# Optimization experiments

Hardware: AMD Instinct MI355X
Metric: run time of the kernel (lower is better)

Reference implementation:

```python
import jax, jax.numpy as jnp
import numpy as np

B, S, D = 2, 2048, 2048
HQ, HKV, HD = 16, 8, 128
F = 8192
V = 32000
L = 2
SW = 512
SOFTCAP = 50.0
THETA = 10000.0
EPS = 1e-6
LAYER_TYPES = ("sliding_attention", "full_attention")
SCALE = HD ** -0.5


def _rms_norm(x, w):
    # Gemma-style RMSNorm: fp32 compute, (1 + weight) scale
    x32 = x.astype(jnp.float32)
    n = x32 * jax.lax.rsqrt(jnp.mean(x32 * x32, axis=-1, keepdims=True) + EPS)
    return (n * (1.0 + w.astype(jnp.float32))).astype(x.dtype)


def _rotate_half(x):
    x1, x2 = jnp.split(x, 2, axis=-1)
    return jnp.concatenate([-x2, x1], axis=-1)


def _rope_cos_sin(position_ids):
    inv_freq = 1.0 / (THETA ** (jnp.arange(0, HD, 2, dtype=jnp.float32) / HD))  # [HD/2]
    freqs = position_ids.astype(jnp.float32)[..., None] * inv_freq  # [B,S,HD/2]
    emb = jnp.concatenate([freqs, freqs], axis=-1)  # [B,S,HD]
    return jnp.cos(emb), jnp.sin(emb)


def _apply_rope(q, k, cos, sin):
    # q,k: [B,H,S,HD]; cos,sin: [B,S,HD] -> unsqueeze head dim
    c, s = cos[:, None], sin[:, None]
    return q * c + _rotate_half(q) * s, k * c + _rotate_half(k) * s


def _build_masks(attention_mask, position_ids):
    key_mask = attention_mask.astype(bool)  # [B,S]
    # segment ids from position resets (packed sequences)
    boundaries = (position_ids[:, 1:] <= position_ids[:, :-1]).astype(jnp.int32)
    seg = jnp.cumsum(jnp.concatenate([jnp.ones((B, 1), jnp.int32), boundaries], axis=1), axis=1)
    block = seg[:, :, None] == seg[:, None, :]  # [B,S,S]
    full = (key_mask[:, None, :] & block)[:, None]  # [B,1,S,S]
    rows = jnp.arange(S)
    dist = rows[:, None] - rows[None, :]
    left = (SW + 1) // 2
    right = SW // 2 + 1
    window = ((dist >= 0) & (dist < left)) | ((dist < 0) & (-dist < right))
    sliding = full & window[None, None]
    return {"full_attention": full, "sliding_attention": sliding}


def _attention(x, l, wq, wk, wv, wo, q_norm_w, k_norm_w, cos, sin, mask):
    q = jnp.einsum("bsd,dhe->bhse", x, wq[l].reshape(D, HQ, HD))
    k = jnp.einsum("bsd,dhe->bhse", x, wk[l].reshape(D, HKV, HD))
    v = jnp.einsum("bsd,dhe->bhse", x, wv[l].reshape(D, HKV, HD))
    q = _rms_norm(q, q_norm_w[l])
    k = _rms_norm(k, k_norm_w[l])
    q, k = _apply_rope(q, k, cos, sin)
    rep = HQ // HKV
    k = jnp.repeat(k, rep, axis=1)  # repeat_kv
    v = jnp.repeat(v, rep, axis=1)
    scores = jnp.einsum("bhqd,bhkd->bhqk", q, k) * SCALE
    scores = jnp.tanh(scores / SOFTCAP) * SOFTCAP  # logit softcapping
    big_neg = jnp.finfo(jnp.float32).min
    scores = jnp.where(mask, scores, big_neg)
    probs = jax.nn.softmax(scores.astype(jnp.float32), axis=-1).astype(x.dtype)
    out = jnp.einsum("bhqk,bhkd->bhqd", probs, v)
    out = out.transpose(0, 2, 1, 3).reshape(B, S, HQ * HD)
    return out @ wo[l]


def _mlp(x, l, w_gate_up, w_down):
    gu = x @ w_gate_up[l]
    gate, up = jnp.split(gu, 2, axis=-1)
    return (jax.nn.gelu(gate, approximate=True) * up) @ w_down[l]


def setup_inputs() -> dict:
    key = jax.random.key(0)
    ks = jax.random.split(key, 12)
    w = lambda k, shape: (jax.random.normal(k, shape, jnp.float32) * 0.02)
    inp = {
        "embed": w(ks[0], (V, D)),
        "wq": w(ks[1], (L, D, HQ * HD)),
        "wk": w(ks[2], (L, D, HKV * HD)),
        "wv": w(ks[3], (L, D, HKV * HD)),
        "wo": w(ks[4], (L, HQ * HD, D)),
        "q_norm_w": jnp.zeros((L, HD), jnp.float32),
        "k_norm_w": jnp.zeros((L, HD), jnp.float32),
        "ln_in": jnp.zeros((L, D), jnp.float32),
        "ln_post_attn": jnp.zeros((L, D), jnp.float32),
        "ln_pre_ffn": jnp.zeros((L, D), jnp.float32),
        "ln_post_ffn": jnp.zeros((L, D), jnp.float32),
        "w_gate_up": w(ks[5], (L, D, 2 * F)),
        "w_down": w(ks[6], (L, F, D)),
        "final_norm_w": jnp.zeros((D,), jnp.float32),
        "input_ids": jax.random.randint(ks[7], (B, S), 0, V, jnp.int32),
        "attention_mask": jnp.ones((B, S), jnp.int32),
        # packed sequences: positions reset at the midpoint of each row
        "position_ids": jnp.broadcast_to(
            jnp.concatenate([jnp.arange(S // 2), jnp.arange(S - S // 2)]).astype(jnp.int32)[None, :],
            (B, S),
        ),
    }
    return inp


def reference(embed, wq, wk, wv, wo, q_norm_w, k_norm_w, ln_in, ln_post_attn,
              ln_pre_ffn, ln_post_ffn, w_gate_up, w_down, final_norm_w,
              input_ids, attention_mask, position_ids):
    masks = _build_masks(attention_mask, position_ids)
    cos, sin = _rope_cos_sin(position_ids)
    # scaled word embedding (Gemma style)
    x = embed[input_ids] * jnp.asarray(D ** 0.5, embed.dtype)
    for l in range(L):
        mask = masks[LAYER_TYPES[l]]
        h = _rms_norm(x, ln_in[l])
        h = _attention(h, l, wq, wk, wv, wo, q_norm_w, k_norm_w, cos, sin, mask)
        x = x + _rms_norm(h, ln_post_attn[l])
        h = _rms_norm(x, ln_pre_ffn[l])
        h = _mlp(h, l, w_gate_up, w_down)
        x = x + _rms_norm(h, ln_post_ffn[l])
    return _rms_norm(x, final_norm_w)
```

## Files before the change

### kernel.cpp

```cpp
#include <hip/hip_runtime.h>
#include <cstdint>
#include <cstddef>

typedef __bf16 bf16x8 __attribute__((ext_vector_type(8)));
typedef float  f32x4  __attribute__((ext_vector_type(4)));

#define BATCH 2
#define SEQ   2048
#define DMODEL 2048
#define NHQ   16
#define NHKV  8
#define HDIM  128
#define FFDIM 8192
#define NTOK  4096

__device__ __forceinline__ f32x4 mfma16(bf16x8 a, bf16x8 b, f32x4 c) {
    return __builtin_amdgcn_mfma_f32_16x16x32_bf16(a, b, c, 0, 0, 0);
}

__device__ __forceinline__ void gload16(const __bf16* g, __bf16* l) {
    __builtin_amdgcn_global_load_lds(
        (const __attribute__((address_space(1))) void*)g,
        (__attribute__((address_space(3))) void*)l, 16, 0, 0);
}

__device__ inline float wave_sum64(float v) {
    v += __shfl_xor(v, 1);  v += __shfl_xor(v, 2);  v += __shfl_xor(v, 4);
    v += __shfl_xor(v, 8);  v += __shfl_xor(v, 16); v += __shfl_xor(v, 32);
    return v;
}

__device__ inline float block_sum256(float v, float* lds4) {
    v = wave_sum64(v);
    const int w = threadIdx.x >> 6;
    __syncthreads();
    if ((threadIdx.x & 63) == 0) lds4[w] = v;
    __syncthreads();
    return lds4[0] + lds4[1] + lds4[2] + lds4[3];
}

__device__ __forceinline__ float softcap_exp(float s_raw) {
    const float K1 = 0.08838834764831845f * 0.04f;
    float u = __expf(s_raw * K1);
    return __expf(50.f - 100.f * __builtin_amdgcn_rcpf(1.f + u));
}

__global__ void transpose_cvt(const float* __restrict__ src, __bf16* __restrict__ dst,
                              int K, int N) {
    __shared__ float tile[32][33];
    const int tx = threadIdx.x, ty = threadIdx.y;
    const int n0 = blockIdx.x * 32, k0 = blockIdx.y * 32;
    #pragma unroll
    for (int i = 0; i < 4; ++i)
        tile[ty + i * 8][tx] = src[(size_t)(k0 + ty + i * 8) * N + n0 + tx];
    __syncthreads();
    #pragma unroll
    for (int i = 0; i < 4; ++i)
        dst[(size_t)(n0 + ty + i * 8) * K + k0 + tx] = (__bf16)tile[tx][ty + i * 8];
}

__global__ void transpose_bf16_k(const __bf16* __restrict__ src0, __bf16* __restrict__ dst0,
                                 int R, int C) {
    __shared__ __bf16 tile[32][34];
    const int z = blockIdx.z;
    const __bf16* src = src0 + (size_t)z * R * C;
    __bf16* dst = dst0 + (size_t)z * R * C;
    const int tx = threadIdx.x, ty = threadIdx.y;
    const int c0 = blockIdx.x * 32, r0 = blockIdx.y * 32;
    #pragma unroll
    for (int i = 0; i < 4; ++i)
        tile[ty + i * 8][tx] = src[(size_t)(r0 + ty + i * 8) * C + c0 + tx];
    __syncthreads();
    #pragma unroll
    for (int i = 0; i < 4; ++i)
        dst[(size_t)(c0 + ty + i * 8) * R + r0 + tx] = tile[tx][ty + i * 8];
}

__global__ __launch_bounds__(256) void embed_k(const float* __restrict__ emb,
                                               const int* __restrict__ ids,
                                               float* __restrict__ x) {
    const int row = blockIdx.x, t = threadIdx.x;
    const int id = ids[row];
    const size_t src = (size_t)id * DMODEL, dst = (size_t)row * DMODEL;
    const float sc = 45.2548339959390f;
    float4 a = *(const float4*)&emb[src + t * 4];
    float4 b = *(const float4*)&emb[src + t * 4 + 1024];
    a.x *= sc; a.y *= sc; a.z *= sc; a.w *= sc;
    b.x *= sc; b.y *= sc; b.z *= sc; b.w *= sc;
    *(float4*)&x[dst + t * 4] = a;
    *(float4*)&x[dst + t * 4 + 1024] = b;
}

__global__ __launch_bounds__(256) void seg_scan(const int* __restrict__ pos,
                                                int* __restrict__ seg) {
    __shared__ int wsum[4];
    const int b = blockIdx.x, t = threadIdx.x;
    const int lane = t & 63, wv = t >> 6;
    const int base = b * SEQ;
    int f[8]; int loc = 0;
    #pragma unroll
    for (int i = 0; i < 8; ++i) {
        int s = t * 8 + i;
        int fl = (s > 0) ? (pos[base + s] <= pos[base + s - 1]) : 0;
        f[i] = fl; loc += fl;
    }
    int sc = loc;
    for (int o = 1; o < 64; o <<= 1) { int n = __shfl_up(sc, o); if (lane >= o) sc += n; }
    if (lane == 63) wsum[wv] = sc;
    __syncthreads();
    int wb = 0;
    for (int i = 0; i < wv; ++i) wb += wsum[i];
    int run = wb + sc - loc + 1;
    #pragma unroll
    for (int i = 0; i < 8; ++i) { run += f[i]; seg[base + t * 8 + i] = run; }
}

template<int MODE, int NH>
__global__ __launch_bounds__(256) void fused_norm_k(
        float* __restrict__ x, const float* __restrict__ hA, const float* __restrict__ hB,
        const float* __restrict__ wA, const float* __restrict__ wB,
        __bf16* __restrict__ outb, float* __restrict__ outf) {
    __shared__ float lds4[4];
    const int row = blockIdx.x, t = threadIdx.x;
    const size_t base = (size_t)row * DMODEL;
    const int c0 = t * 4, c1 = t * 4 + 1024;
    float v[8];
    if constexpr (MODE == 0) {
        float4 a = *(const float4*)&x[base + c0];
        float4 b = *(const float4*)&x[base + c1];
        v[0]=a.x; v[1]=a.y; v[2]=a.z; v[3]=a.w;
        v[4]=b.x; v[5]=b.y; v[6]=b.z; v[7]=b.w;
    } else {
        float4 ha = *(const float4*)&hA[base + c0];
        float4 hb = *(const float4*)&hA[base + c1];
        float hv[8] = {ha.x, ha.y, ha.z, ha.w, hb.x, hb.y, hb.z, hb.w};
        if constexpr (NH == 2) {
            float4 ga = *(const float4*)&hB[base + c0];
            float4 gb = *(const float4*)&hB[base + c1];
            hv[0]+=ga.x; hv[1]+=ga.y; hv[2]+=ga.z; hv[3]+=ga.w;
            hv[4]+=gb.x; hv[5]+=gb.y; hv[6]+=gb.z; hv[7]+=gb.w;
        }
        float ss = 0.f;
        #pragma unroll
        for (int i = 0; i < 8; ++i) ss += hv[i] * hv[i];
        float tot = block_sum256(ss, lds4);
        float rs = rsqrtf(tot * (1.f / DMODEL) + 1e-6f);
        float4 xa = *(const float4*)&x[base + c0];
        float4 xb = *(const float4*)&x[base + c1];
        float xv[8] = {xa.x, xa.y, xa.z, xa.w, xb.x, xb.y, xb.z, xb.w};
        #pragma unroll
        for (int i = 0; i < 8; ++i) {
            int c = (i < 4) ? c0 + i : c1 + i - 4;
            v[i] = xv[i] + hv[i] * rs * (1.f + wA[c]);
        }
        float4 o0 = {v[0], v[1], v[2], v[3]}, o1 = {v[4], v[5], v[6], v[7]};
        *(float4*)&x[base + c0] = o0;
        *(float4*)&x[base + c1] = o1;
    }
    float ss2 = 0.f;
    #pragma unroll
    for (int i = 0; i < 8; ++i) ss2 += v[i] * v[i];
    float tot2 = block_sum256(ss2, lds4);
    float rs2 = rsqrtf(tot2 * (1.f / DMODEL) + 1e-6f);
    #pragma unroll
    for (int i = 0; i < 8; ++i) {
        int c = (i < 4) ? c0 + i : c1 + i - 4;
        float o = v[i] * rs2 * (1.f + wB[c]);
        if constexpr (MODE == 2) outf[base + c] = o;
        else outb[base + c] = (__bf16)o;
    }
}

template<int MH, int NH>
__device__ __forceinline__ void quad(f32x4 (&acc)[8][4], const bf16x8 (&af)[4][2],
                                     const bf16x8 (&bfr)[2][2]) {
    #pragma unroll
    for (int mq = 0; mq < 4; ++mq)
        #pragma unroll
        for (int nq = 0; nq < 2; ++nq)
            #pragma unroll
            for (int ks = 0; ks < 2; ++ks)
                acc[MH*4+mq][NH*2+nq] = mfma16(af[mq][ks], bfr[nq][ks], acc[MH*4+mq][NH*2+nq]);
}

template<typename OutT>
__global__ __launch_bounds__(512, 2) void gemm8p(const __bf16* __restrict__ A,
                                                 const __bf16* __restrict__ Bw,
                                                 OutT* __restrict__ C,
                                                 int M, int N, int Ksub, int lda, int ldb) {
    __shared__ __bf16 lds[65536];
    const int z = blockIdx.z;
    A += (size_t)z * Ksub;
    Bw += (size_t)z * Ksub;
    C += (size_t)z * M * N;

    const int nx = gridDim.x;
    const int nwg = nx * gridDim.y;
    const int orig = blockIdx.y * nx + blockIdx.x;
    const int wg = ((nwg & 7) == 0) ? ((orig & 7) * (nwg >> 3) + (orig >> 3)) : orig;
    const int bm = (wg / nx) * 256;
    const int bn = (wg % nx) * 256;

    const int t = threadIdx.x;
    const int w = t >> 6, lane = t & 63;
    const int wm = w >> 2, wn = w & 3;
    const int lg = lane >> 4, lr = lane & 15;

    const int rS = t >> 3, sS = t & 7;
    const int colS = ((sS ^ (rS & 7)) << 3);
    const __bf16* Ag = A + (size_t)(bm + rS) * lda + colS;
    const __bf16* Bg = Bw + (size_t)(bn + rS) * ldb + colS;
    const int nt = Ksub >> 6;

#define STAGE_A(kt, h) { \
        const __bf16* g_ = Ag + (size_t)(h) * 128 * lda + (size_t)(kt) * 64; \
        const int li_ = (((kt) & 1) << 15) + ((h) << 13) + t * 8; \
        gload16(g_, &lds[li_]); \
        gload16(g_ + (size_t)64 * lda, &lds[li_ + 4096]); }
#define STAGE_B(kt, h) { \
        const __bf16* g_ = Bg + (size_t)(h) * 128 * ldb + (size_t)(kt) * 64; \
        const int li_ = (((kt) & 1) << 15) + 16384 + ((h) << 13) + t * 8; \
        gload16(g_, &lds[li_]); \
        gload16(g_ + (size_t)64 * ldb, &lds[li_ + 4096]); }

    f32x4 acc[8][4] = {};
    bf16x8 af[4][2], bf0[2][2], bf1[2][2];

    const int swz = (lr & 7) << 3;
    const int aBase = wm * 8192;
    const int bBase = 16384 + (wn >> 1) * 8192;
    const int bRow0 = (wn & 1) * 64;

    STAGE_A(0, 0); STAGE_A(0, 1); STAGE_B(0, 0); STAGE_B(0, 1);
    if (nt > 1) {
        STAGE_A(1, 0); STAGE_A(1, 1);
        asm volatile("s_waitcnt vmcnt(4)" ::: "memory");
    } else {
        asm volatile("s_waitcnt vmcnt(0)" ::: "memory");
    }
    __builtin_amdgcn_s_barrier();
    asm volatile("" ::: "memory");

    for (int kt = 0; kt < nt; ++kt) {
        const int buf = (kt & 1) << 15;
        const bool p1 = (kt + 1 < nt), p2 = (kt + 2 < nt);
        #pragma unroll
        for (int mq = 0; mq < 4; ++mq)
            #pragma unroll
            for (int ks = 0; ks < 2; ++ks)
                af[mq][ks] = *(const bf16x8*)&lds[buf + aBase + (((mq*16 + lr)*64 + ks*32 + lg*8) ^ swz)];
        #pragma unroll
        for (int nq = 0; nq < 2; ++nq)
            #pragma unroll
            for (int ks = 0; ks < 2; ++ks)
                bf0[nq][ks] = *(const bf16x8*)&lds[buf + bBase + (((bRow0 + nq*16 + lr)*64 + ks*32 + lg*8) ^ swz)];
        __builtin_amdgcn_sched_barrier(0);
        if (p1) STAGE_B(kt + 1, 0);
        __builtin_amdgcn_s_barrier();
        asm volatile("s_waitcnt lgkmcnt(0)" ::: "memory");
        __builtin_amdgcn_sched_barrier(0);
        __builtin_amdgcn_s_setprio(1);
        quad<0,0>(acc, af, bf0);
        __builtin_amdgcn_s_setprio(0);
        __builtin_amdgcn_s_barrier();
        asm volatile("" ::: "memory");
        #pragma unroll
        for (int nq = 0; nq < 2; ++nq)
            #pragma unroll
            for (int ks = 0; ks < 2; ++ks)
                bf1[nq][ks] = *(const bf16x8*)&lds[buf + bBase + (((bRow0 + 32 + nq*16 + lr)*64 + ks*32 + lg*8) ^ swz)];
        __builtin_amdgcn_sched_barrier(0);
        if (p1) STAGE_B(kt + 1, 1);
        __builtin_amdgcn_s_barrier();
        asm volatile("s_waitcnt lgkmcnt(0)" ::: "memory");
        __builtin_amdgcn_sched_barrier(0);
        __builtin_amdgcn_s_setprio(1);
        quad<0,1>(acc, af, bf1);
        __builtin_amdgcn_s_setprio(0);
        __builtin_amdgcn_s_barrier();
        asm volatile("" ::: "memory");
        #pragma unroll
        for (int mq = 0; mq < 4; ++mq)
            #pragma unroll
            for (int ks = 0; ks < 2; ++ks)
                af[mq][ks] = *(const bf16x8*)&lds[buf + aBase + (((64 + mq*16 + lr)*64 + ks*32 + lg*8) ^ swz)];
        __builtin_amdgcn_sched_barrier(0);
        __builtin_amdgcn_s_barrier();
        asm volatile("s_waitcnt lgkmcnt(0)" ::: "memory");
        __builtin_amdgcn_sched_barrier(0);
        __builtin_amdgcn_s_setprio(1);
        quad<1,1>(acc, af, bf1);
        __builtin_amdgcn_s_setprio(0);
        __builtin_amdgcn_s_barrier();
        asm volatile("" ::: "memory");
        if (p2) {
            STAGE_A(kt + 2, 0); STAGE_A(kt + 2, 1);
            asm volatile("s_waitcnt vmcnt(4)" ::: "memory");
        } else if (p1) {
            asm volatile("s_waitcnt vmcnt(0)" ::: "memory");
        }
        __builtin_amdgcn_s_barrier();
        __builtin_amdgcn_sched_barrier(0);
        __builtin_amdgcn_s_setprio(1);
        quad<1,0>(acc, af, bf0);
        __builtin_amdgcn_s_setprio(0);
        __builtin_amdgcn_s_barrier();
        asm volatile("" ::: "memory");
    }
#undef STAGE_A
#undef STAGE_B

    #pragma unroll
    for (int m = 0; m < 8; ++m)
        #pragma unroll
        for (int n = 0; n < 4; ++n)
            #pragma unroll
            for (int r = 0; r < 4; ++r) {
                const int row = bm + wm * 128 + m * 16 + lg * 4 + r;
                const int col = bn + wn * 64 + n * 16 + lr;
                C[(size_t)row * N + col] = (OutT)acc[m][n][r];
            }
}

__global__ __launch_bounds__(256) void reduce4(const float* __restrict__ p,
                                               float* __restrict__ out, int n) {
    const int i = (blockIdx.x * 256 + threadIdx.x) * 4;
    float4 a = *(const float4*)&p[i];
    float4 b = *(const float4*)&p[i + n];
    float4 c = *(const float4*)&p[i + 2 * (size_t)n];
    float4 d = *(const float4*)&p[i + 3 * (size_t)n];
    float4 r = {a.x+b.x+c.x+d.x, a.y+b.y+c.y+d.y, a.z+b.z+c.z+d.z, a.w+b.w+c.w+d.w};
    *(float4*)&out[i] = r;
}

__global__ __launch_bounds__(256) void qkv_post(const __bf16* __restrict__ qkv,
                                                const float* __restrict__ qnw,
                                                const float* __restrict__ knw,
                                                const int* __restrict__ posid,
                                                __bf16* __restrict__ qg,
                                                __bf16* __restrict__ kg,
                                                __bf16* __restrict__ vg) {
    const int slot = blockIdx.x * 4 + (threadIdx.x >> 6);
    const int lane = threadIdx.x & 63;
    const int token = slot >> 5, j = slot & 31;
    const int b = token >> 11, s = token & (SEQ - 1);
    int base;
    const float* nw = nullptr;
    if (j < 16)      { base = j * 128;                nw = qnw; }
    else if (j < 24) { base = 2048 + (j - 16) * 128;  nw = knw; }
    else             { base = 3072 + (j - 24) * 128; }
    float e0 = (float)qkv[(size_t)token * 4096 + base + lane];
    float e1 = (float)qkv[(size_t)token * 4096 + base + lane + 64];
    if (j < 24) {
        float ss = wave_sum64(e0 * e0 + e1 * e1);
        float rs = rsqrtf(ss * (1.f / 128.f) + 1e-6f);
        e0 *= rs * (1.f + nw[lane]);
        e1 *= rs * (1.f + nw[lane + 64]);
        float p = (float)posid[token];
        float inv = exp2f(-13.287712379549449f * ((float)lane * (1.f / 64.f)));
        float f = p * inv;
        float c = cosf(f), sn = sinf(f);
        float o0 = e0 * c - e1 * sn;
        float o1 = e1 * c + e0 * sn;
        e0 = o0; e1 = o1;
    }
    size_t dst; __bf16* out;
    if (j < 16)      { dst = ((size_t)(b * NHQ  + j)        * SEQ + s) * HDIM; out = qg; }
    else if (j < 24) { dst = ((size_t)(b * NHKV + (j - 16)) * SEQ + s) * HDIM; out = kg; }
    else             { dst = ((size_t)(b * NHKV + (j - 24)) * SEQ + s) * HDIM; out = vg; }
    out[dst + lane] = (__bf16)e0;
    out[dst + lane + 64] = (__bf16)e1;
}

template<int SLIDING>
__global__ __launch_bounds__(256, 2) void attn_k(const __bf16* __restrict__ qg,
                                                 const __bf16* __restrict__ kg,
                                                 const __bf16* __restrict__ vtg,
                                                 const int* __restrict__ seg,
                                                 const int* __restrict__ amask,
                                                 __bf16* __restrict__ outg) {
    __shared__ __align__(16) __bf16 Ks[64][136];
    __shared__ __align__(16) __bf16 Vs[128][72];
    __shared__ __align__(16) __bf16 Ps[4][16][72];
    __shared__ int segq_s[64], segk_s[64], kmk_s[64];
    __shared__ int flag_s;
    const int bh = blockIdx.y;
    const int b = bh >> 4, h = bh & 15, kvh = h >> 1;
    const int qb = blockIdx.x * 64;
    const int t = threadIdx.x, w = t >> 6, lane = t & 63;
    const int lg = lane >> 4, lr = lane & 15;
    const int segbase = b * SEQ;

    const size_t qoff = ((size_t)(b * NHQ + h) * SEQ + qb + w * 16) * HDIM;
    bf16x8 qf[4];
    #pragma unroll
    for (int kk = 0; kk < 4; ++kk)
        qf[kk] = *(const bf16x8*)&qg[qoff + (size_t)lr * HDIM + kk * 32 + lg * 8];
    if (t < 64) segq_s[t] = seg[segbase + qb + t];

    const int sqmin = seg[segbase + qb], sqmax = seg[segbase + qb + 63];

    const int krow = t >> 4, kcol = (t & 15) * 8;
    const int vrow = t >> 3, vcol = (t & 7) * 8;
    const __bf16* kB = kg + ((size_t)(b * NHKV + kvh) * SEQ) * HDIM + (size_t)krow * HDIM + kcol;
    const __bf16* vB = vtg + ((size_t)(b * NHKV + kvh) * HDIM + vrow) * SEQ + vcol;

    auto chunk_active = [&](int kb) -> bool {
        if (SLIDING && (qb - kb < -318 || qb - kb > 319)) return false;
        int skmin = seg[segbase + kb], skmax = seg[segbase + kb + 63];
        return (skmax >= sqmin) && (skmin <= sqmax);
    };
    auto next_kb = [&](int kb) -> int {
        for (kb += 64; kb < SEQ; kb += 64)
            if (chunk_active(kb)) return kb;
        return SEQ;
    };

    int4 kr0, kr1, kr2, kr3, vr0, vr1, vr2, vr3;
#define LOADR(kb_) { \
        kr0 = *(const int4*)(kB + (size_t)(kb_) * HDIM); \
        kr1 = *(const int4*)(kB + (size_t)((kb_) + 16) * HDIM); \
        kr2 = *(const int4*)(kB + (size_t)((kb_) + 32) * HDIM); \
        kr3 = *(const int4*)(kB + (size_t)((kb_) + 48) * HDIM); \
        vr0 = *(const int4*)(vB + (kb_)); \
        vr1 = *(const int4*)(vB + (size_t)32 * SEQ + (kb_)); \
        vr2 = *(const int4*)(vB + (size_t)64 * SEQ + (kb_)); \
        vr3 = *(const int4*)(vB + (size_t)96 * SEQ + (kb_)); }

    f32x4 oacc[8] = {};
    float den[4] = {0.f, 0.f, 0.f, 0.f};

    int kb = chunk_active(0) ? 0 : next_kb(0);
    if (kb < SEQ) LOADR(kb);

    while (kb < SEQ) {
        const int nkb = next_kb(kb);
        __syncthreads();
        *(int4*)&Ks[krow     ][kcol] = kr0;
        *(int4*)&Ks[krow + 16][kcol] = kr1;
        *(int4*)&Ks[krow + 32][kcol] = kr2;
        *(int4*)&Ks[krow + 48][kcol] = kr3;
        *(int4*)&Vs[vrow     ][vcol] = vr0;
        *(int4*)&Vs[vrow + 32][vcol] = vr1;
        *(int4*)&Vs[vrow + 64][vcol] = vr2;
        *(int4*)&Vs[vrow + 96][vcol] = vr3;
        if (w == 0) {
            int m = amask[segbase + kb + lane];
            int sk = seg[segbase + kb + lane];
            kmk_s[lane] = m; segk_s[lane] = sk;
            bool allm = (__ballot(m != 0) == ~0ull);
            bool segu = __all(sk == sqmin) && (sqmin == sqmax);
            bool wall = !SLIDING || (qb - kb >= -193 && qb - kb <= 192);
            if (lane == 0) flag_s = (allm && segu && wall) ? 1 : 0;
        }
        __syncthreads();
        if (nkb < SEQ) LOADR(nkb);
        const bool fast = (flag_s != 0);

        #pragma unroll
        for (int n = 0; n < 4; ++n) {
            f32x4 sc = {};
            #pragma unroll
            for (int kk = 0; kk < 4; ++kk) {
                bf16x8 bfr = *(const bf16x8*)&Ks[n * 16 + lr][kk * 32 + lg * 8];
                sc = mfma16(qf[kk], bfr, sc);
            }
            if (fast) {
                #pragma unroll
                for (int r = 0; r < 4; ++r) {
                    int row = lg * 4 + r;
                    float p = softcap_exp(sc[r]);
                    den[r] += p;
                    Ps[w][row][n * 16 + lr] = (__bf16)p;
                }
            } else {
                #pragma unroll
                for (int r = 0; r < 4; ++r) {
                    int row = lg * 4 + r;
                    int qi = qb + w * 16 + row;
                    int ki = kb + n * 16 + lr;
                    bool ok = (kmk_s[n * 16 + lr] != 0) &&
                              (segq_s[w * 16 + row] == segk_s[n * 16 + lr]);
                    if (SLIDING) { int d = qi - ki; ok = ok && (d >= -256) && (d <= 255); }
                    float p = ok ? softcap_exp(sc[r]) : 0.f;
                    den[r] += p;
                    Ps[w][row][n * 16 + lr] = (__bf16)p;
                }
            }
        }
        #pragma unroll
        for (int kk2 = 0; kk2 < 2; ++kk2) {
            bf16x8 pf = *(const bf16x8*)&Ps[w][lr][kk2 * 32 + lg * 8];
            #pragma unroll
            for (int n2 = 0; n2 < 8; ++n2) {
                bf16x8 vf = *(const bf16x8*)&Vs[n2 * 16 + lr][kk2 * 32 + lg * 8];
                oacc[n2] = mfma16(pf, vf, oacc[n2]);
            }
        }
        kb = nkb;
    }
#undef LOADR
    #pragma unroll
    for (int r = 0; r < 4; ++r) {
        float v = den[r];
        v += __shfl_xor(v, 1); v += __shfl_xor(v, 2);
        v += __shfl_xor(v, 4); v += __shfl_xor(v, 8);
        den[r] = __builtin_amdgcn_rcpf(v);
    }
    #pragma unroll
    for (int n2 = 0; n2 < 8; ++n2)
        #pragma unroll
        for (int r = 0; r < 4; ++r) {
            int row = qb + w * 16 + lg * 4 + r;
            float val = oacc[n2][r] * den[r];
            outg[((size_t)(b * SEQ) + row) * DMODEL + h * HDIM + n2 * 16 + lr] = (__bf16)val;
        }
}

__global__ __launch_bounds__(256) void gelu_mul(const __bf16* __restrict__ gu,
                                                __bf16* __restrict__ act) {
    const int idx = blockIdx.x * 256 + threadIdx.x;
    const int r = idx >> 10;
    const int c = (idx & 1023) * 8;
    bf16x8 g8 = *(const bf16x8*)&gu[(size_t)r * 16384 + c];
    bf16x8 u8 = *(const bf16x8*)&gu[(size_t)r * 16384 + 8192 + c];
    bf16x8 res;
    #pragma unroll
    for (int i = 0; i < 8; ++i) {
        float g = (float)g8[i], u = (float)u8[i];
        float a = 0.7978845608028654f * (g + 0.044715f * g * g * g);
        float ge = 0.5f * g * (1.f + tanhf(a));
        res[i] = (__bf16)(ge * u);
    }
    *(bf16x8*)&act[(size_t)r * 8192 + c] = res;
}

extern "C" void kernel_launch(void* const* d_in, const int* in_sizes, int n_in,
                              void* d_out, int out_size, void* d_ws, size_t ws_size,
                              hipStream_t stream) {
    const float* embedw = (const float*)d_in[0];
    const float* wq   = (const float*)d_in[1];
    const float* wk   = (const float*)d_in[2];
    const float* wv   = (const float*)d_in[3];
    const float* wo   = (const float*)d_in[4];
    const float* qnw  = (const float*)d_in[5];
    const float* knw  = (const float*)d_in[6];
    const float* lnin = (const float*)d_in[7];
    const float* lnpa = (const float*)d_in[8];
    const float* lnpf = (const float*)d_in[9];
    const float* lnpff= (const float*)d_in[10];
    const float* wguW = (const float*)d_in[11];
    const float* wdnW = (const float*)d_in[12];
    const float* fnw  = (const float*)d_in[13];
    const int* ids    = (const int*)d_in[14];
    const int* amask  = (const int*)d_in[15];
    const int* posid  = (const int*)d_in[16];
    float* outp = (float*)d_out;

    char* ws = (char*)d_ws;
    size_t off = 0;
    auto A = [&](size_t b) -> char* {
        char* p = ws + off;
        off = (off + b + 255) & ~(size_t)255;
        return p;
    };
    __bf16* qkvwt = (__bf16*)A((size_t)4096 * 2048 * 2);
    __bf16* wot   = (__bf16*)A((size_t)2048 * 2048 * 2);
    __bf16* wgut  = (__bf16*)A((size_t)16384 * 2048 * 2);
    __bf16* wdnt  = (__bf16*)A((size_t)2048 * 8192 * 2);
    float*  x     = (float*)A((size_t)NTOK * DMODEL * 4);
    __bf16* hbuf  = (__bf16*)A((size_t)NTOK * DMODEL * 2);
    char*   big   = A((size_t)NTOK * 4096 * 4);
    __bf16* qkvb  = (__bf16*)big;
    __bf16* gubuf = (__bf16*)big;
    __bf16* qbh   = (__bf16*)A((size_t)BATCH * NHQ  * SEQ * HDIM * 2);
    __bf16* kbh   = (__bf16*)A((size_t)BATCH * NHKV * SEQ * HDIM * 2);
    __bf16* vbh   = (__bf16*)A((size_t)BATCH * NHKV * SEQ * HDIM * 2);
    __bf16* vtbh  = (__bf16*)A((size_t)BATCH * NHKV * SEQ * HDIM * 2);
    __bf16* attnb = (__bf16*)A((size_t)NTOK * DMODEL * 2);
    float*  h2    = (float*)A((size_t)NTOK * DMODEL * 4);
    __bf16* actb  = (__bf16*)A((size_t)2048 * FFDIM * 2);
    float*  pbuf  = (float*)A((size_t)4 * 2048 * 2048 * 4);
    int*    seg   = (int*)A((size_t)BATCH * SEQ * 4);
    if (off > ws_size) return;

    const dim3 tb(32, 8);
    seg_scan<<<BATCH, 256, 0, stream>>>(posid, seg);
    embed_k<<<NTOK, 256, 0, stream>>>(embedw, ids, x);
    fused_norm_k<0,1><<<NTOK, 256, 0, stream>>>(x, nullptr, nullptr, nullptr, lnin, hbuf, nullptr);

    for (int l = 0; l < 2; ++l) {
        transpose_cvt<<<dim3(64, 64), tb, 0, stream>>>(wq + (size_t)l * 2048 * 2048,
            qkvwt, 2048, 2048);
        transpose_cvt<<<dim3(32, 64), tb, 0, stream>>>(wk + (size_t)l * 2048 * 1024,
            qkvwt + (size_t)2048 * 2048, 2048, 1024);
        transpose_cvt<<<dim3(32, 64), tb, 0, stream>>>(wv + (size_t)l * 2048 * 1024,
            qkvwt + (size_t)3072 * 2048, 2048, 1024);
        transpose_cvt<<<dim3(64, 64), tb, 0, stream>>>(wo + (size_t)l * 2048 * 2048,
            wot, 2048, 2048);
        transpose_cvt<<<dim3(512, 64), tb, 0, stream>>>(wguW + (size_t)l * 2048 * 16384,
            wgut, 2048, 16384);
        transpose_cvt<<<dim3(64, 256), tb, 0, stream>>>(wdnW + (size_t)l * 8192 * 2048,
            wdnt, 8192, 2048);

        gemm8p<__bf16><<<dim3(16, 16, 1), 512, 0, stream>>>(hbuf, qkvwt, qkvb,
                                                            4096, 4096, 2048, 2048, 2048);
        qkv_post<<<32768, 256, 0, stream>>>(qkvb, qnw + l * 128, knw + l * 128, posid,
                                            qbh, kbh, vbh);
        transpose_bf16_k<<<dim3(4, 64, BATCH * NHKV), tb, 0, stream>>>(vbh, vtbh, SEQ, HDIM);
        if (l == 0)
            attn_k<1><<<dim3(SEQ / 64, BATCH * NHQ), 256, 0, stream>>>(qbh, kbh, vtbh, seg,
                                                                       amask, attnb);
        else
            attn_k<0><<<dim3(SEQ / 64, BATCH * NHQ), 256, 0, stream>>>(qbh, kbh, vtbh, seg,
                                                                       amask, attnb);
        gemm8p<float><<<dim3(8, 16, 2), 512, 0, stream>>>(attnb, wot, pbuf,
                                                          4096, 2048, 1024, 2048, 2048);
        fused_norm_k<1,2><<<NTOK, 256, 0, stream>>>(x, pbuf, pbuf + (size_t)4096 * 2048,
                                                    lnpa + l * 2048, lnpf + l * 2048,
                                                    hbuf, nullptr);
        for (int c = 0; c < 2; ++c) {
            gemm8p<__bf16><<<dim3(64, 8, 1), 512, 0, stream>>>(
                hbuf + (size_t)c * 2048 * 2048, wgut, gubuf, 2048, 16384, 2048, 2048, 2048);
            gelu_mul<<<8192, 256, 0, stream>>>(gubuf, actb);
            gemm8p<float><<<dim3(8, 8, 4), 512, 0, stream>>>(actb, wdnt, pbuf,
                                                             2048, 2048, 2048, 8192, 8192);
            reduce4<<<4096, 256, 0, stream>>>(pbuf, h2 + (size_t)c * 2048 * 2048, 2048 * 2048);
        }
        if (l == 0)
            fused_norm_k<1,1><<<NTOK, 256, 0, stream>>>(x, h2, nullptr, lnpff, lnin + 2048,
                                                        hbuf, nullptr);
        else
            fused_norm_k<2,1><<<NTOK, 256, 0, stream>>>(x, h2, nullptr, lnpff + 2048, fnw,
                                                        nullptr, outp);
    }
}
```

Baseline: 1.651 ms.

## Fuse GELU-gate multiply into gate/up GEMM epilogue via interleaved weight columns

The gate/up weight transpose now interleaves gate and up rows so adjacent output columns hold a gate/up pair. The GEMM epilogue pairs lanes with a shuffle, computes tanh-GELU in its sigmoid form, multiplies by the up value, and writes half-width bf16 activations directly. This removes the separate gelu_mul kernel and the round trip of the 2048x16384 intermediate through global memory. The cost is extra epilogue math, stores from only half the lanes, and a different gelu formulation that may shift numerics slightly.

```diff
diff --git a/kernel.cpp b/kernel.cpp
--- a/kernel.cpp
+++ b/kernel.cpp
@@ -57,6 +57,23 @@
     #pragma unroll
     for (int i = 0; i < 4; ++i)
         dst[(size_t)(n0 + ty + i * 8) * K + k0 + tx] = (__bf16)tile[tx][ty + i * 8];
+}
+
+__global__ void transpose_cvt_gu(const float* __restrict__ src, __bf16* __restrict__ dst,
+                                 int K, int N) {
+    __shared__ float tile[32][33];
+    const int tx = threadIdx.x, ty = threadIdx.y;
+    const int n0 = blockIdx.x * 32, k0 = blockIdx.y * 32;
+    #pragma unroll
+    for (int i = 0; i < 4; ++i)
+        tile[ty + i * 8][tx] = src[(size_t)(k0 + ty + i * 8) * N + n0 + tx];
+    __syncthreads();
+    #pragma unroll
+    for (int i = 0; i < 4; ++i) {
+        int n = n0 + ty + i * 8;
+        int rI = (n < 8192) ? (2 * n) : (2 * (n - 8192) + 1);
+        dst[(size_t)rI * K + k0 + tx] = (__bf16)tile[tx][ty + i * 8];
+    }
 }
 
 __global__ void transpose_bf16_k(const __bf16* __restrict__ src0, __bf16* __restrict__ dst0,
@@ -183,7 +200,7 @@
                 acc[MH*4+mq][NH*2+nq] = mfma16(af[mq][ks], bfr[nq][ks], acc[MH*4+mq][NH*2+nq]);
 }
 
-template<typename OutT>
+template<typename OutT, int GELU>
 __global__ __launch_bounds__(512, 2) void gemm8p(const __bf16* __restrict__ A,
                                                  const __bf16* __restrict__ Bw,
                                                  OutT* __restrict__ C,
@@ -310,16 +327,37 @@
 #undef STAGE_A
 #undef STAGE_B
 
-    #pragma unroll
-    for (int m = 0; m < 8; ++m)
-        #pragma unroll
-        for (int n = 0; n < 4; ++n)
-            #pragma unroll
-            for (int r = 0; r < 4; ++r) {
-                const int row = bm + wm * 128 + m * 16 + lg * 4 + r;
-                const int col = bn + wn * 64 + n * 16 + lr;
-                C[(size_t)row * N + col] = (OutT)acc[m][n][r];
-            }
+    if constexpr (GELU) {
+        const int nhalf = N >> 1;
+        #pragma unroll
+        for (int m = 0; m < 8; ++m)
+            #pragma unroll
+            for (int n = 0; n < 4; ++n)
+                #pragma unroll
+                for (int r = 0; r < 4; ++r) {
+                    float v = acc[m][n][r];
+                    float p = __shfl_xor(v, 1);
+                    float a2 = 1.5957691216057308f * (v + 0.044715f * v * v * v);
+                    float sig = __builtin_amdgcn_rcpf(1.f + __expf(-a2));
+                    float res = v * sig * p;
+                    if (!(lane & 1)) {
+                        const int row = bm + wm * 128 + m * 16 + lg * 4 + r;
+                        const int col = (bn >> 1) + wn * 32 + n * 8 + (lr >> 1);
+                        C[(size_t)row * nhalf + col] = (OutT)res;
+                    }
+                }
+    } else {
+        #pragma unroll
+        for (int m = 0; m < 8; ++m)
+            #pragma unroll
+            for (int n = 0; n < 4; ++n)
+                #pragma unroll
+                for (int r = 0; r < 4; ++r) {
+                    const int row = bm + wm * 128 + m * 16 + lg * 4 + r;
+                    const int col = bn + wn * 64 + n * 16 + lr;
+                    C[(size_t)row * N + col] = (OutT)acc[m][n][r];
+                }
+    }
 }
 
 __global__ __launch_bounds__(256) void reduce4(const float* __restrict__ p,
@@ -517,24 +555,6 @@
         }
 }
 
-__global__ __launch_bounds__(256) void gelu_mul(const __bf16* __restrict__ gu,
-                                                __bf16* __restrict__ act) {
-    const int idx = blockIdx.x * 256 + threadIdx.x;
-    const int r = idx >> 10;
-    const int c = (idx & 1023) * 8;
-    bf16x8 g8 = *(const bf16x8*)&gu[(size_t)r * 16384 + c];
-    bf16x8 u8 = *(const bf16x8*)&gu[(size_t)r * 16384 + 8192 + c];
-    bf16x8 res;
-    #pragma unroll
-    for (int i = 0; i < 8; ++i) {
-        float g = (float)g8[i], u = (float)u8[i];
-        float a = 0.7978845608028654f * (g + 0.044715f * g * g * g);
-        float ge = 0.5f * g * (1.f + tanhf(a));
-        res[i] = (__bf16)(ge * u);
-    }
-    *(bf16x8*)&act[(size_t)r * 8192 + c] = res;
-}
-
 extern "C" void kernel_launch(void* const* d_in, const int* in_sizes, int n_in,
                               void* d_out, int out_size, void* d_ws, size_t ws_size,
                               hipStream_t stream) {
@@ -570,9 +590,7 @@
     __bf16* wdnt  = (__bf16*)A((size_t)2048 * 8192 * 2);
     float*  x     = (float*)A((size_t)NTOK * DMODEL * 4);
     __bf16* hbuf  = (__bf16*)A((size_t)NTOK * DMODEL * 2);
-    char*   big   = A((size_t)NTOK * 4096 * 4);
-    __bf16* qkvb  = (__bf16*)big;
-    __bf16* gubuf = (__bf16*)big;
+    __bf16* qkvb  = (__bf16*)A((size_t)NTOK * 4096 * 2);
     __bf16* qbh   = (__bf16*)A((size_t)BATCH * NHQ  * SEQ * HDIM * 2);
     __bf16* kbh   = (__bf16*)A((size_t)BATCH * NHKV * SEQ * HDIM * 2);
     __bf16* vbh   = (__bf16*)A((size_t)BATCH * NHKV * SEQ * HDIM * 2);
@@ -598,13 +616,13 @@
             qkvwt + (size_t)3072 * 2048, 2048, 1024);
         transpose_cvt<<<dim3(64, 64), tb, 0, stream>>>(wo + (size_t)l * 2048 * 2048,
             wot, 2048, 2048);
-        transpose_cvt<<<dim3(512, 64), tb, 0, stream>>>(wguW + (size_t)l * 2048 * 16384,
+        transpose_cvt_gu<<<dim3(512, 64), tb, 0, stream>>>(wguW + (size_t)l * 2048 * 16384,
             wgut, 2048, 16384);
         transpose_cvt<<<dim3(64, 256), tb, 0, stream>>>(wdnW + (size_t)l * 8192 * 2048,
             wdnt, 8192, 2048);
 
-        gemm8p<__bf16><<<dim3(16, 16, 1), 512, 0, stream>>>(hbuf, qkvwt, qkvb,
-                                                            4096, 4096, 2048, 2048, 2048);
+        gemm8p<__bf16,0><<<dim3(16, 16, 1), 512, 0, stream>>>(hbuf, qkvwt, qkvb,
+                                                              4096, 4096, 2048, 2048, 2048);
         qkv_post<<<32768, 256, 0, stream>>>(qkvb, qnw + l * 128, knw + l * 128, posid,
                                             qbh, kbh, vbh);
         transpose_bf16_k<<<dim3(4, 64, BATCH * NHKV), tb, 0, stream>>>(vbh, vtbh, SEQ, HDIM);
@@ -614,17 +632,16 @@
         else
             attn_k<0><<<dim3(SEQ / 64, BATCH * NHQ), 256, 0, stream>>>(qbh, kbh, vtbh, seg,
                                                                        amask, attnb);
-        gemm8p<float><<<dim3(8, 16, 2), 512, 0, stream>>>(attnb, wot, pbuf,
-                                                          4096, 2048, 1024, 2048, 2048);
+        gemm8p<float,0><<<dim3(8, 16, 2), 512, 0, stream>>>(attnb, wot, pbuf,
+                                                            4096, 2048, 1024, 2048, 2048);
         fused_norm_k<1,2><<<NTOK, 256, 0, stream>>>(x, pbuf, pbuf + (size_t)4096 * 2048,
                                                     lnpa + l * 2048, lnpf + l * 2048,
                                                     hbuf, nullptr);
         for (int c = 0; c < 2; ++c) {
-            gemm8p<__bf16><<<dim3(64, 8, 1), 512, 0, stream>>>(
-                hbuf + (size_t)c * 2048 * 2048, wgut, gubuf, 2048, 16384, 2048, 2048, 2048);
-            gelu_mul<<<8192, 256, 0, stream>>>(gubuf, actb);
-            gemm8p<float><<<dim3(8, 8, 4), 512, 0, stream>>>(actb, wdnt, pbuf,
-                                                             2048, 2048, 2048, 8192, 8192);
+            gemm8p<__bf16,1><<<dim3(64, 8, 1), 512, 0, stream>>>(
+                hbuf + (size_t)c * 2048 * 2048, wgut, actb, 2048, 16384, 2048, 2048, 2048);
+            gemm8p<float,0><<<dim3(8, 8, 4), 512, 0, stream>>>(actb, wdnt, pbuf,
+                                                               2048, 2048, 2048, 8192, 8192);
             reduce4<<<4096, 256, 0, stream>>>(pbuf, h2 + (size_t)c * 2048 * 2048, 2048 * 2048);
         }
         if (l == 0)
```

New measurement: 1.604 ms. -2.8%, faster.
